# Kernel optimization log

Hardware: AMD Instinct MI355X
Metric: run time of the kernel (lower is better)

## Reference

```python
import jax, jax.numpy as jnp
import numpy as np

N_NODES = 100000
N_EDGES = 1600000
FEATURE = 128
HIDDEN = 128
CLASSES = 64


def _sage_conv(x, src, dst, W_l, b_l, W_r, num_nodes):
    # mean aggregation of source-node features at destination nodes
    msgs = x[src]                                            # [E, F]
    agg = jax.ops.segment_sum(msgs, dst, num_segments=num_nodes)   # [N, F]
    cnt = jax.ops.segment_sum(jnp.ones((src.shape[0],), x.dtype), dst,
                              num_segments=num_nodes)        # [N]
    mean = agg / jnp.maximum(cnt, 1.0)[:, None]              # zero for isolated nodes
    return mean @ W_l.T + b_l + x @ W_r.T


def setup_inputs() -> dict:
    key = jax.random.key(0)
    ks = jax.random.split(key, 8)
    x = jax.random.normal(ks[0], (N_NODES, FEATURE), dtype=jnp.float32)
    edge_index = jax.random.randint(ks[1], (2, N_EDGES), 0, N_NODES, dtype=jnp.int64)
    s1 = 1.0 / np.sqrt(FEATURE)
    s2 = 1.0 / np.sqrt(HIDDEN)
    W1l = jax.random.uniform(ks[2], (HIDDEN, FEATURE), jnp.float32, -s1, s1)
    b1l = jnp.zeros((HIDDEN,), jnp.float32)
    W1r = jax.random.uniform(ks[3], (HIDDEN, FEATURE), jnp.float32, -s1, s1)
    W2l = jax.random.uniform(ks[4], (CLASSES, HIDDEN), jnp.float32, -s2, s2)
    b2l = jnp.zeros((CLASSES,), jnp.float32)
    W2r = jax.random.uniform(ks[5], (CLASSES, HIDDEN), jnp.float32, -s2, s2)
    return {"x": x, "edge_index": edge_index,
            "W1l": W1l, "b1l": b1l, "W1r": W1r,
            "W2l": W2l, "b2l": b2l, "W2r": W2r}


def reference(x, edge_index, W1l, b1l, W1r, W2l, b2l, W2r):
    src, dst = edge_index[0], edge_index[1]
    h = _sage_conv(x, src, dst, W1l, b1l, W1r, N_NODES)
    h = jax.nn.relu(h)
    # F.dropout(training=False) is identity in eval mode
    out = _sage_conv(h, src, dst, W2l, b2l, W2r, N_NODES)
    return jax.nn.log_softmax(out, axis=1)
```

## Files before the change

### kernel.cpp

```cpp
#include <hip/hip_runtime.h>

#define NF 128
#define NC 64
#define NBA 640
#define NBKT 196

typedef short short8 __attribute__((ext_vector_type(8)));
typedef unsigned short ushort;
typedef float f32x4 __attribute__((ext_vector_type(4)));
typedef float f32x2 __attribute__((ext_vector_type(2)));
typedef unsigned int uint;
typedef unsigned char uchar;

__device__ __forceinline__ ushort f2b(float x) {
  unsigned u = __builtin_bit_cast(unsigned, x);
  u += 0x7fffu + ((u >> 16) & 1u);
  return (ushort)(u >> 16);
}

__global__ void prep_kernel(const float* __restrict__ x, ushort* __restrict__ xb,
                            uchar* __restrict__ x8, int n4, int nb_cast,
                            const float* __restrict__ W1l, const float* __restrict__ W1r,
                            ushort* __restrict__ Wp1,
                            const float* __restrict__ W2l, const float* __restrict__ W2r,
                            ushort* __restrict__ Wp2l, ushort* __restrict__ Wp2r) {
  int b = blockIdx.x;
  if (b < nb_cast) {
    int i = b * 256 + threadIdx.x;
    if (i >= n4) return;
    float4 v = ((const float4*)x)[i];
    ushort4 o;
    o.x = f2b(v.x); o.y = f2b(v.y); o.z = f2b(v.z); o.w = f2b(v.w);
    ((ushort4*)xb)[i] = o;
    int u = __builtin_amdgcn_cvt_pk_fp8_f32(v.x, v.y, 0, false);
    u = __builtin_amdgcn_cvt_pk_fp8_f32(v.z, v.w, u, true);
    ((uint*)x8)[i] = (uint)u;
  } else if (b < nb_cast + 128) {
    int tid = (b - nb_cast) * 256 + threadIdx.x;
    int j = tid & 7;
    int lane = (tid >> 3) & 63;
    int tile = tid >> 9;
    int nt = tile & 7, kt = tile >> 3;
    int k = kt * 32 + ((lane >> 4) << 3) + j;
    int n = nt * 16 + (lane & 15);
    float v = (k < 128) ? W1l[n * 128 + k] : W1r[n * 128 + (k - 128)];
    Wp1[tid] = f2b(v);
  } else {
    int tid0 = (b - nb_cast - 128) * 256 + threadIdx.x;
    int which = tid0 >> 13;
    int tid = tid0 & 8191;
    int j = tid & 7;
    int lane = (tid >> 3) & 63;
    int tile = tid >> 9;
    int nt = tile & 3, kt = tile >> 2;
    int k = kt * 32 + ((lane >> 4) << 3) + j;
    int n = nt * 16 + (lane & 15);
    const float* W = which ? W2r : W2l;
    ushort* Wp = which ? Wp2r : Wp2l;
    Wp[tid] = f2b(W[n * 128 + k]);
  }
}

__global__ __launch_bounds__(256) void bhistA_kernel(const int* __restrict__ dst,
                                                     int* __restrict__ cntA,
                                                     int nE, int epb) {
  __shared__ int lh[NBKT];
  const int t = threadIdx.x;
  for (int i = t; i < NBKT; i += 256) lh[i] = 0;
  __syncthreads();
  int s0 = blockIdx.x * epb, s1 = min(nE, s0 + epb);
  for (int e = s0 + t; e < s1; e += 256) atomicAdd(&lh[dst[e] >> 9], 1);
  __syncthreads();
  for (int i = t; i < NBKT; i += 256)
    cntA[(size_t)i * NBA + blockIdx.x] = lh[i];
}

__global__ __launch_bounds__(256) void scanL1_kernel(const int* __restrict__ in,
                                                     int* __restrict__ out,
                                                     int* __restrict__ bsum, int L) {
  const int t = threadIdx.x;
  const int base = blockIdx.x * 1024 + t * 4;
  int v[4];
  int tsum = 0;
#pragma unroll
  for (int k = 0; k < 4; ++k) {
    v[k] = (base + k < L) ? in[base + k] : 0;
    tsum += v[k];
  }
  int lane = t & 63, wid = t >> 6;
  int x = tsum;
#pragma unroll
  for (int d = 1; d < 64; d <<= 1) {
    int y = __shfl_up(x, d);
    if (lane >= d) x += y;
  }
  __shared__ int wsum[4];
  if (lane == 63) wsum[wid] = x;
  __syncthreads();
  int wbase = 0;
  for (int w = 0; w < wid; ++w) wbase += wsum[w];
  int run = wbase + x - tsum;
#pragma unroll
  for (int k = 0; k < 4; ++k) {
    if (base + k < L) out[base + k] = run;
    run += v[k];
  }
  if (t == 0) bsum[blockIdx.x] = wsum[0] + wsum[1] + wsum[2] + wsum[3];
}

__global__ void scanL2_kernel(int* __restrict__ bsum, int nb) {
  int lane = threadIdx.x;
  int i0 = 2 * lane, i1 = 2 * lane + 1;
  int v0 = (i0 < nb) ? bsum[i0] : 0;
  int v1 = (i1 < nb) ? bsum[i1] : 0;
  int s = v0 + v1;
  int x = s;
#pragma unroll
  for (int d = 1; d < 64; d <<= 1) {
    int y = __shfl_up(x, d);
    if (lane >= d) x += y;
  }
  int ex = x - s;
  if (i0 < nb) bsum[i0] = ex;
  if (i1 < nb) bsum[i1] = ex + v0;
}

__global__ void scanL3_kernel(int* __restrict__ out, const int* __restrict__ bsum, int L) {
  int i = blockIdx.x * blockDim.x + threadIdx.x;
  if (i < L) out[i] += bsum[i >> 10];
}

__global__ __launch_bounds__(256) void bscatA_kernel(const int* __restrict__ src,
                                                     const int* __restrict__ dst,
                                                     const int* __restrict__ cntS,
                                                     uint* __restrict__ tmp,
                                                     int nE, int epb) {
  __shared__ int base[NBKT];
  __shared__ int cur[NBKT];
  const int t = threadIdx.x;
  for (int i = t; i < NBKT; i += 256) {
    base[i] = cntS[(size_t)i * NBA + blockIdx.x];
    cur[i] = 0;
  }
  __syncthreads();
  int s0 = blockIdx.x * epb, s1 = min(nE, s0 + epb);
  for (int e = s0 + t; e < s1; e += 256) {
    int d = dst[e];
    int s = src[e];
    int b = d >> 9;
    int r = atomicAdd(&cur[b], 1);
    tmp[base[b] + r] = ((uint)(d & 511) << 17) | (uint)s;
  }
}

__global__ __launch_bounds__(256) void bsortB_kernel(const uint* __restrict__ tmp,
                                                     const int* __restrict__ cntS,
                                                     int* __restrict__ esrc,
                                                     int* __restrict__ deg,
                                                     int* __restrict__ off,
                                                     int nN, int nE) {
  const int bkt = blockIdx.x;
  const int t = threadIdx.x;
  __shared__ int lh[512];
  __shared__ int cur[512];
  __shared__ int wsum[4];
  const int start = cntS[(size_t)bkt * NBA];
  const int end = (bkt + 1 < NBKT) ? cntS[(size_t)(bkt + 1) * NBA] : nE;
  lh[t] = 0;
  lh[t + 256] = 0;
  __syncthreads();
  for (int i = start + t; i < end; i += 256) {
    uint e = tmp[i];
    atomicAdd(&lh[e >> 17], 1);
  }
  __syncthreads();
  int v0 = lh[2 * t], v1 = lh[2 * t + 1];
  int ts = v0 + v1;
  int lane = t & 63, wid = t >> 6;
  int x = ts;
#pragma unroll
  for (int d = 1; d < 64; d <<= 1) {
    int y = __shfl_up(x, d);
    if (lane >= d) x += y;
  }
  if (lane == 63) wsum[wid] = x;
  __syncthreads();
  int wb = 0;
  for (int w = 0; w < wid; ++w) wb += wsum[w];
  int ex = wb + x - ts;
  cur[2 * t] = ex;
  cur[2 * t + 1] = ex + v0;
  int n0 = (bkt << 9) + 2 * t, n1 = n0 + 1;
  if (n0 < nN) { off[n0] = start + ex;      deg[n0] = v0; }
  if (n1 < nN) { off[n1] = start + ex + v0; deg[n1] = v1; }
  __syncthreads();
  for (int i = start + t; i < end; i += 256) {
    uint e = tmp[i];
    int r = atomicAdd(&cur[e >> 17], 1);
    esrc[start + r] = (int)(e & 0x1FFFFu);
  }
}

__global__ __launch_bounds__(256) void gather1_kernel(
    const uchar* __restrict__ x8, const int* __restrict__ esrc,
    const int* __restrict__ off, const int* __restrict__ deg,
    ushort* __restrict__ aggm, int nN) {
  const int w = (blockIdx.x * blockDim.x + threadIdx.x) >> 6;
  const int lane = threadIdx.x & 63;
  if (w >= nN) return;
  const int o = off[w];
  const int d = deg[w];
  const int g = lane >> 4;
  const int l = lane & 15;
  f32x2 acc[4] = {};
  int i = 0;
  for (; i + 8 <= d; i += 8) {
    int sA = esrc[o + i + g];
    int sB = esrc[o + i + 4 + g];
    uint2 vA = ((const uint2*)(x8 + (size_t)sA * NF))[l];
    uint2 vB = ((const uint2*)(x8 + (size_t)sB * NF))[l];
    acc[0] += __builtin_amdgcn_cvt_pk_f32_fp8(vA.x, false) +
              __builtin_amdgcn_cvt_pk_f32_fp8(vB.x, false);
    acc[1] += __builtin_amdgcn_cvt_pk_f32_fp8(vA.x, true) +
              __builtin_amdgcn_cvt_pk_f32_fp8(vB.x, true);
    acc[2] += __builtin_amdgcn_cvt_pk_f32_fp8(vA.y, false) +
              __builtin_amdgcn_cvt_pk_f32_fp8(vB.y, false);
    acc[3] += __builtin_amdgcn_cvt_pk_f32_fp8(vA.y, true) +
              __builtin_amdgcn_cvt_pk_f32_fp8(vB.y, true);
  }
  for (; i + 4 <= d; i += 4) {
    int s = esrc[o + i + g];
    uint2 v = ((const uint2*)(x8 + (size_t)s * NF))[l];
    acc[0] += __builtin_amdgcn_cvt_pk_f32_fp8(v.x, false);
    acc[1] += __builtin_amdgcn_cvt_pk_f32_fp8(v.x, true);
    acc[2] += __builtin_amdgcn_cvt_pk_f32_fp8(v.y, false);
    acc[3] += __builtin_amdgcn_cvt_pk_f32_fp8(v.y, true);
  }
  if (i + g < d) {
    int s = esrc[o + i + g];
    uint2 v = ((const uint2*)(x8 + (size_t)s * NF))[l];
    acc[0] += __builtin_amdgcn_cvt_pk_f32_fp8(v.x, false);
    acc[1] += __builtin_amdgcn_cvt_pk_f32_fp8(v.x, true);
    acc[2] += __builtin_amdgcn_cvt_pk_f32_fp8(v.y, false);
    acc[3] += __builtin_amdgcn_cvt_pk_f32_fp8(v.y, true);
  }
  float r[8];
#pragma unroll
  for (int k = 0; k < 4; ++k) { r[2 * k] = acc[k].x; r[2 * k + 1] = acc[k].y; }
#pragma unroll
  for (int k = 0; k < 8; ++k) {
    r[k] += __shfl_xor(r[k], 16);
    r[k] += __shfl_xor(r[k], 32);
  }
  if (g == 0) {
    float inv = 1.0f / fmaxf((float)d, 1.0f);
    uint4 ov;
    ov.x = (uint)f2b(r[0] * inv) | ((uint)f2b(r[1] * inv) << 16);
    ov.y = (uint)f2b(r[2] * inv) | ((uint)f2b(r[3] * inv) << 16);
    ov.z = (uint)f2b(r[4] * inv) | ((uint)f2b(r[5] * inv) << 16);
    ov.w = (uint)f2b(r[6] * inv) | ((uint)f2b(r[7] * inv) << 16);
    ((uint4*)(aggm + (size_t)w * NF))[l] = ov;
  }
}

__global__ __launch_bounds__(256) void gather2_kernel(
    const uchar* __restrict__ z8, const int* __restrict__ esrc,
    const int* __restrict__ off, const int* __restrict__ deg,
    float* __restrict__ aggz, int nN) {
  const int w = (blockIdx.x * blockDim.x + threadIdx.x) >> 6;
  const int lane = threadIdx.x & 63;
  if (w >= nN) return;
  const int o = off[w];
  const int d = deg[w];
  const int g = lane >> 4;
  const int l = lane & 15;
  f32x2 acc[2] = {};
  int i = 0;
  for (; i + 8 <= d; i += 8) {
    int sA = esrc[o + i + g];
    int sB = esrc[o + i + 4 + g];
    uint vA = ((const uint*)(z8 + (size_t)sA * NC))[l];
    uint vB = ((const uint*)(z8 + (size_t)sB * NC))[l];
    acc[0] += __builtin_amdgcn_cvt_pk_f32_fp8(vA, false) +
              __builtin_amdgcn_cvt_pk_f32_fp8(vB, false);
    acc[1] += __builtin_amdgcn_cvt_pk_f32_fp8(vA, true) +
              __builtin_amdgcn_cvt_pk_f32_fp8(vB, true);
  }
  for (; i + 4 <= d; i += 4) {
    int s = esrc[o + i + g];
    uint v = ((const uint*)(z8 + (size_t)s * NC))[l];
    acc[0] += __builtin_amdgcn_cvt_pk_f32_fp8(v, false);
    acc[1] += __builtin_amdgcn_cvt_pk_f32_fp8(v, true);
  }
  if (i + g < d) {
    int s = esrc[o + i + g];
    uint v = ((const uint*)(z8 + (size_t)s * NC))[l];
    acc[0] += __builtin_amdgcn_cvt_pk_f32_fp8(v, false);
    acc[1] += __builtin_amdgcn_cvt_pk_f32_fp8(v, true);
  }
  float r[4] = {acc[0].x, acc[0].y, acc[1].x, acc[1].y};
#pragma unroll
  for (int k = 0; k < 4; ++k) {
    r[k] += __shfl_xor(r[k], 16);
    r[k] += __shfl_xor(r[k], 32);
  }
  if (g == 0) {
    float inv = 1.0f / fmaxf((float)d, 1.0f);
    ((float4*)(aggz + (size_t)w * NC))[l] =
        make_float4(r[0] * inv, r[1] * inv, r[2] * inv, r[3] * inv);
  }
}

__global__ __launch_bounds__(256) void layer1_mfma(
    const ushort* __restrict__ xb, const ushort* __restrict__ aggb,
    const ushort* __restrict__ Wp, const float* __restrict__ b1,
    ushort* __restrict__ hb, int nN) {
  const int t = threadIdx.x;
  const int wv = t >> 6;
  const int lane = t & 63;
  const int base = blockIdx.x * 64;
  __shared__ ushort As[64][264];
  for (int i = t; i < 64 * 32; i += 256) {
    int r = i >> 5, cq = i & 31;
    int node = base + r;
    short8 v = {};
    if (node < nN) {
      const ushort* sp = (cq < 16) ? (aggb + (size_t)node * NF + cq * 8)
                                   : (xb + (size_t)node * NF + (cq - 16) * 8);
      v = *(const short8*)sp;
    }
    *(short8*)&As[r][cq * 8] = v;
  }
  __syncthreads();

  f32x4 acc[8] = {};
  const int arow = wv * 16 + (lane & 15);
  const int kq = (lane >> 4) * 8;
#pragma unroll
  for (int kt = 0; kt < 8; ++kt) {
    short8 af = *(const short8*)&As[arow][kt * 32 + kq];
#pragma unroll
    for (int nt = 0; nt < 8; ++nt) {
      short8 bf = *(const short8*)(Wp + ((size_t)(kt * 8 + nt) * 64 + lane) * 8);
      acc[nt] = __builtin_amdgcn_mfma_f32_16x16x32_bf16(af, bf, acc[nt], 0, 0, 0);
    }
  }
  const int quad = lane >> 4;
  const int cl = lane & 15;
#pragma unroll
  for (int nt = 0; nt < 8; ++nt) {
    float bj = b1[nt * 16 + cl];
#pragma unroll
    for (int r = 0; r < 4; ++r) {
      int node = base + wv * 16 + quad * 4 + r;
      if (node < nN) {
        float vv = fmaxf(acc[nt][r] + bj, 0.0f);
        hb[(size_t)node * NF + nt * 16 + cl] = f2b(vv);
      }
    }
  }
}

__global__ __launch_bounds__(256) void layer2a_mfma(
    const ushort* __restrict__ hb, const ushort* __restrict__ Wp,
    uchar* __restrict__ z8, int nN) {
  const int t = threadIdx.x;
  const int wv = t >> 6;
  const int lane = t & 63;
  const int base = blockIdx.x * 64;
  __shared__ ushort As[64][136];
  for (int i = t; i < 64 * 16; i += 256) {
    int r = i >> 4, cq = i & 15;
    int node = base + r;
    short8 v = {};
    if (node < nN) v = *(const short8*)(hb + (size_t)node * NF + cq * 8);
    *(short8*)&As[r][cq * 8] = v;
  }
  __syncthreads();

  f32x4 acc[4] = {};
  const int arow = wv * 16 + (lane & 15);
  const int kq = (lane >> 4) * 8;
#pragma unroll
  for (int kt = 0; kt < 4; ++kt) {
    short8 af = *(const short8*)&As[arow][kt * 32 + kq];
#pragma unroll
    for (int nt = 0; nt < 4; ++nt) {
      short8 bf = *(const short8*)(Wp + ((size_t)(kt * 4 + nt) * 64 + lane) * 8);
      acc[nt] = __builtin_amdgcn_mfma_f32_16x16x32_bf16(af, bf, acc[nt], 0, 0, 0);
    }
  }
  const int quad = lane >> 4;
  const int cl = lane & 15;
#pragma unroll
  for (int r = 0; r < 4; ++r) {
    int node = base + wv * 16 + quad * 4 + r;
    if (node < nN) {
      int u = __builtin_amdgcn_cvt_pk_fp8_f32(acc[0][r], acc[1][r], 0, false);
      u = __builtin_amdgcn_cvt_pk_fp8_f32(acc[2][r], acc[3][r], u, true);
      ((uint*)(z8 + (size_t)node * NC))[cl] = (uint)u;
    }
  }
}

__global__ __launch_bounds__(256) void layer2b_mfma(
    const ushort* __restrict__ hb, const float* __restrict__ aggz,
    const ushort* __restrict__ Wp, const float* __restrict__ b2,
    float* __restrict__ out, int nN) {
  const int t = threadIdx.x;
  const int wv = t >> 6;
  const int lane = t & 63;
  const int base = blockIdx.x * 64;
  __shared__ ushort As[64][136];
  for (int i = t; i < 64 * 16; i += 256) {
    int r = i >> 4, cq = i & 15;
    int node = base + r;
    short8 v = {};
    if (node < nN) v = *(const short8*)(hb + (size_t)node * NF + cq * 8);
    *(short8*)&As[r][cq * 8] = v;
  }
  __syncthreads();

  f32x4 acc[4] = {};
  const int arow = wv * 16 + (lane & 15);
  const int kq = (lane >> 4) * 8;
#pragma unroll
  for (int kt = 0; kt < 4; ++kt) {
    short8 af = *(const short8*)&As[arow][kt * 32 + kq];
#pragma unroll
    for (int nt = 0; nt < 4; ++nt) {
      short8 bf = *(const short8*)(Wp + ((size_t)(kt * 4 + nt) * 64 + lane) * 8);
      acc[nt] = __builtin_amdgcn_mfma_f32_16x16x32_bf16(af, bf, acc[nt], 0, 0, 0);
    }
  }
  const int quad = lane >> 4;
  const int cl = lane & 15;
  float bj[4];
#pragma unroll
  for (int nt = 0; nt < 4; ++nt) bj[nt] = b2[nt * 16 + cl];

#pragma unroll
  for (int r = 0; r < 4; ++r) {
    int node = base + wv * 16 + quad * 4 + r;
    int nvalid = (node < nN);
    float a0 = 0.f, a1 = 0.f, a2 = 0.f, a3 = 0.f;
    if (nvalid) {
      float4 av = ((const float4*)(aggz + (size_t)node * NC))[cl];
      a0 = av.x; a1 = av.y; a2 = av.z; a3 = av.w;
    }
    float v0 = acc[0][r] + bj[0] + a0;
    float v1 = acc[1][r] + bj[1] + a1;
    float v2 = acc[2][r] + bj[2] + a2;
    float v3 = acc[3][r] + bj[3] + a3;
    float mx = fmaxf(fmaxf(v0, v1), fmaxf(v2, v3));
#pragma unroll
    for (int s = 1; s < 16; s <<= 1) mx = fmaxf(mx, __shfl_xor(mx, s));
    float sm = expf(v0 - mx) + expf(v1 - mx) + expf(v2 - mx) + expf(v3 - mx);
#pragma unroll
    for (int s = 1; s < 16; s <<= 1) sm += __shfl_xor(sm, s);
    float ls = mx + logf(sm);
    if (nvalid) {
      float* op = out + (size_t)node * NC;
      op[0 * 16 + cl] = v0 - ls;
      op[1 * 16 + cl] = v1 - ls;
      op[2 * 16 + cl] = v2 - ls;
      op[3 * 16 + cl] = v3 - ls;
    }
  }
}

extern "C" void kernel_launch(void* const* d_in, const int* in_sizes, int n_in,
                              void* d_out, int out_size, void* d_ws, size_t ws_size,
                              hipStream_t stream) {
  const float* x   = (const float*)d_in[0];
  const int*   ei  = (const int*)d_in[1];
  const float* W1l = (const float*)d_in[2];
  const float* b1l = (const float*)d_in[3];
  const float* W1r = (const float*)d_in[4];
  const float* W2l = (const float*)d_in[5];
  const float* b2l = (const float*)d_in[6];
  const float* W2r = (const float*)d_in[7];
  float* out = (float*)d_out;

  const int nN = in_sizes[0] / NF;
  const int nE = in_sizes[1] / 2;
  const int* src = ei;
  const int* dst = ei + nE;

  char* p = (char*)d_ws;
  ushort* xb   = (ushort*)p; p += (size_t)nN * NF * 2;
  ushort* hb   = (ushort*)p; p += (size_t)nN * NF * 2;
  ushort* aggb = (ushort*)p; p += (size_t)nN * NF * 2;
  ushort* Wp1  = (ushort*)p; p += 256 * 128 * 2;
  ushort* Wp2l = (ushort*)p; p += 128 * 64 * 2;
  ushort* Wp2r = (ushort*)p; p += 128 * 64 * 2;
  int* cntA = (int*)p; p += (size_t)NBKT * NBA * 4;
  int* cntS = (int*)p; p += (size_t)NBKT * NBA * 4;
  int* bsum = (int*)p; p += 512;
  int* deg  = (int*)p; p += (size_t)nN * 4;
  int* off  = (int*)p; p += (size_t)nN * 4;
  int* esrc = (int*)p; p += (size_t)nE * 4;
  uint* tmp = (uint*)p; p += (size_t)nE * 4;

  uchar* x8   = (uchar*)hb;
  uchar* z8   = (uchar*)tmp;
  float* aggz = (float*)aggb;

  const int n4 = nN * NF / 4;
  const int nb_cast = (n4 + 255) / 256;
  const int epb = (nE + NBA - 1) / NBA;
  const int L = NBKT * NBA;
  const int nbL = (L + 1023) / 1024;

  prep_kernel<<<nb_cast + 128 + 64, 256, 0, stream>>>(x, xb, x8, n4, nb_cast,
                                                      W1l, W1r, Wp1,
                                                      W2l, W2r, Wp2l, Wp2r);

  bhistA_kernel<<<NBA, 256, 0, stream>>>(dst, cntA, nE, epb);
  scanL1_kernel<<<nbL, 256, 0, stream>>>(cntA, cntS, bsum, L);
  scanL2_kernel<<<1, 64, 0, stream>>>(bsum, nbL);
  scanL3_kernel<<<(L + 255) / 256, 256, 0, stream>>>(cntS, bsum, L);
  bscatA_kernel<<<NBA, 256, 0, stream>>>(src, dst, cntS, tmp, nE, epb);
  bsortB_kernel<<<NBKT, 256, 0, stream>>>(tmp, cntS, esrc, deg, off, nN, nE);

  gather1_kernel<<<(nN + 3) / 4, 256, 0, stream>>>(x8, esrc, off, deg, aggb, nN);
  layer1_mfma<<<(nN + 63) / 64, 256, 0, stream>>>(xb, aggb, Wp1, b1l, hb, nN);

  layer2a_mfma<<<(nN + 63) / 64, 256, 0, stream>>>(hb, Wp2l, z8, nN);
  gather2_kernel<<<(nN + 3) / 4, 256, 0, stream>>>(z8, esrc, off, deg, aggz, nN);
  layer2b_mfma<<<(nN + 63) / 64, 256, 0, stream>>>(hb, aggz, Wp2r, b2l, out, nN);
}
```

Baseline: 316.7 us.

## Fuse histogram into prep, fold scan fixup, widen gathers, fuse layer1 with layer2a

The bucket histogram now runs as extra blocks of the prep kernel. The final scan-add kernel is removed and its block offsets are added where bscatA and bsortB read them. Layer 1 and the layer-2 left projection are fused: the ReLU output is written into LDS and reused for the second MFMA, so hb is not re-read from global memory. Both gather kernels now use 8 lanes per row with wider loads and 16 edges per iteration. Together these cut launch count and global traffic, at the cost of more registers, one extra shuffle stage per reduction, and more shared state in the prep kernel.

```diff
diff --git a/kernel.cpp b/kernel.cpp
--- a/kernel.cpp
+++ b/kernel.cpp
@@ -18,12 +18,15 @@
   return (ushort)(u >> 16);
 }
 
-__global__ void prep_kernel(const float* __restrict__ x, ushort* __restrict__ xb,
-                            uchar* __restrict__ x8, int n4, int nb_cast,
-                            const float* __restrict__ W1l, const float* __restrict__ W1r,
-                            ushort* __restrict__ Wp1,
-                            const float* __restrict__ W2l, const float* __restrict__ W2r,
-                            ushort* __restrict__ Wp2l, ushort* __restrict__ Wp2r) {
+__global__ __launch_bounds__(256) void prep_kernel(
+    const float* __restrict__ x, ushort* __restrict__ xb,
+    uchar* __restrict__ x8, int n4, int nb_cast,
+    const float* __restrict__ W1l, const float* __restrict__ W1r,
+    ushort* __restrict__ Wp1,
+    const float* __restrict__ W2l, const float* __restrict__ W2r,
+    ushort* __restrict__ Wp2l, ushort* __restrict__ Wp2r,
+    const int* __restrict__ dst, int* __restrict__ cntA, int nE, int epb) {
+  __shared__ int lh[NBKT];
   int b = blockIdx.x;
   if (b < nb_cast) {
     int i = b * 256 + threadIdx.x;
@@ -45,7 +48,7 @@
     int n = nt * 16 + (lane & 15);
     float v = (k < 128) ? W1l[n * 128 + k] : W1r[n * 128 + (k - 128)];
     Wp1[tid] = f2b(v);
-  } else {
+  } else if (b < nb_cast + 192) {
     int tid0 = (b - nb_cast - 128) * 256 + threadIdx.x;
     int which = tid0 >> 13;
     int tid = tid0 & 8191;
@@ -58,21 +61,17 @@
     const float* W = which ? W2r : W2l;
     ushort* Wp = which ? Wp2r : Wp2l;
     Wp[tid] = f2b(W[n * 128 + k]);
-  }
-}
-
-__global__ __launch_bounds__(256) void bhistA_kernel(const int* __restrict__ dst,
-                                                     int* __restrict__ cntA,
-                                                     int nE, int epb) {
-  __shared__ int lh[NBKT];
-  const int t = threadIdx.x;
-  for (int i = t; i < NBKT; i += 256) lh[i] = 0;
-  __syncthreads();
-  int s0 = blockIdx.x * epb, s1 = min(nE, s0 + epb);
-  for (int e = s0 + t; e < s1; e += 256) atomicAdd(&lh[dst[e] >> 9], 1);
-  __syncthreads();
-  for (int i = t; i < NBKT; i += 256)
-    cntA[(size_t)i * NBA + blockIdx.x] = lh[i];
+  } else {
+    int blk = b - nb_cast - 192;
+    const int t = threadIdx.x;
+    for (int i = t; i < NBKT; i += 256) lh[i] = 0;
+    __syncthreads();
+    int s0 = blk * epb, s1 = min(nE, s0 + epb);
+    for (int e = s0 + t; e < s1; e += 256) atomicAdd(&lh[dst[e] >> 9], 1);
+    __syncthreads();
+    for (int i = t; i < NBKT; i += 256)
+      cntA[(size_t)i * NBA + blk] = lh[i];
+  }
 }
 
 __global__ __launch_bounds__(256) void scanL1_kernel(const int* __restrict__ in,
@@ -125,21 +124,18 @@
   if (i1 < nb) bsum[i1] = ex + v0;
 }
 
-__global__ void scanL3_kernel(int* __restrict__ out, const int* __restrict__ bsum, int L) {
-  int i = blockIdx.x * blockDim.x + threadIdx.x;
-  if (i < L) out[i] += bsum[i >> 10];
-}
-
 __global__ __launch_bounds__(256) void bscatA_kernel(const int* __restrict__ src,
                                                      const int* __restrict__ dst,
                                                      const int* __restrict__ cntS,
+                                                     const int* __restrict__ bsum,
                                                      uint* __restrict__ tmp,
                                                      int nE, int epb) {
   __shared__ int base[NBKT];
   __shared__ int cur[NBKT];
   const int t = threadIdx.x;
   for (int i = t; i < NBKT; i += 256) {
-    base[i] = cntS[(size_t)i * NBA + blockIdx.x];
+    size_t idx = (size_t)i * NBA + blockIdx.x;
+    base[i] = cntS[idx] + bsum[idx >> 10];
     cur[i] = 0;
   }
   __syncthreads();
@@ -155,6 +151,7 @@
 
 __global__ __launch_bounds__(256) void bsortB_kernel(const uint* __restrict__ tmp,
                                                      const int* __restrict__ cntS,
+                                                     const int* __restrict__ bsum,
                                                      int* __restrict__ esrc,
                                                      int* __restrict__ deg,
                                                      int* __restrict__ off,
@@ -164,8 +161,15 @@
   __shared__ int lh[512];
   __shared__ int cur[512];
   __shared__ int wsum[4];
-  const int start = cntS[(size_t)bkt * NBA];
-  const int end = (bkt + 1 < NBKT) ? cntS[(size_t)(bkt + 1) * NBA] : nE;
+  const size_t ia = (size_t)bkt * NBA;
+  const int start = cntS[ia] + bsum[ia >> 10];
+  int end;
+  if (bkt + 1 < NBKT) {
+    const size_t ib = (size_t)(bkt + 1) * NBA;
+    end = cntS[ib] + bsum[ib >> 10];
+  } else {
+    end = nE;
+  }
   lh[t] = 0;
   lh[t + 256] = 0;
   __syncthreads();
@@ -210,15 +214,15 @@
   if (w >= nN) return;
   const int o = off[w];
   const int d = deg[w];
-  const int g = lane >> 4;
-  const int l = lane & 15;
-  f32x2 acc[4] = {};
+  const int g = lane >> 3;
+  const int l = lane & 7;
+  f32x2 acc[8] = {};
   int i = 0;
-  for (; i + 8 <= d; i += 8) {
+  for (; i + 16 <= d; i += 16) {
     int sA = esrc[o + i + g];
-    int sB = esrc[o + i + 4 + g];
-    uint2 vA = ((const uint2*)(x8 + (size_t)sA * NF))[l];
-    uint2 vB = ((const uint2*)(x8 + (size_t)sB * NF))[l];
+    int sB = esrc[o + i + 8 + g];
+    uint4 vA = ((const uint4*)(x8 + (size_t)sA * NF))[l];
+    uint4 vB = ((const uint4*)(x8 + (size_t)sB * NF))[l];
     acc[0] += __builtin_amdgcn_cvt_pk_f32_fp8(vA.x, false) +
               __builtin_amdgcn_cvt_pk_f32_fp8(vB.x, false);
     acc[1] += __builtin_amdgcn_cvt_pk_f32_fp8(vA.x, true) +
@@ -227,39 +231,61 @@
               __builtin_amdgcn_cvt_pk_f32_fp8(vB.y, false);
     acc[3] += __builtin_amdgcn_cvt_pk_f32_fp8(vA.y, true) +
               __builtin_amdgcn_cvt_pk_f32_fp8(vB.y, true);
-  }
-  for (; i + 4 <= d; i += 4) {
+    acc[4] += __builtin_amdgcn_cvt_pk_f32_fp8(vA.z, false) +
+              __builtin_amdgcn_cvt_pk_f32_fp8(vB.z, false);
+    acc[5] += __builtin_amdgcn_cvt_pk_f32_fp8(vA.z, true) +
+              __builtin_amdgcn_cvt_pk_f32_fp8(vB.z, true);
+    acc[6] += __builtin_amdgcn_cvt_pk_f32_fp8(vA.w, false) +
+              __builtin_amdgcn_cvt_pk_f32_fp8(vB.w, false);
+    acc[7] += __builtin_amdgcn_cvt_pk_f32_fp8(vA.w, true) +
+              __builtin_amdgcn_cvt_pk_f32_fp8(vB.w, true);
+  }
+  for (; i + 8 <= d; i += 8) {
     int s = esrc[o + i + g];
-    uint2 v = ((const uint2*)(x8 + (size_t)s * NF))[l];
+    uint4 v = ((const uint4*)(x8 + (size_t)s * NF))[l];
     acc[0] += __builtin_amdgcn_cvt_pk_f32_fp8(v.x, false);
     acc[1] += __builtin_amdgcn_cvt_pk_f32_fp8(v.x, true);
     acc[2] += __builtin_amdgcn_cvt_pk_f32_fp8(v.y, false);
     acc[3] += __builtin_amdgcn_cvt_pk_f32_fp8(v.y, true);
+    acc[4] += __builtin_amdgcn_cvt_pk_f32_fp8(v.z, false);
+    acc[5] += __builtin_amdgcn_cvt_pk_f32_fp8(v.z, true);
+    acc[6] += __builtin_amdgcn_cvt_pk_f32_fp8(v.w, false);
+    acc[7] += __builtin_amdgcn_cvt_pk_f32_fp8(v.w, true);
   }
   if (i + g < d) {
     int s = esrc[o + i + g];
-    uint2 v = ((const uint2*)(x8 + (size_t)s * NF))[l];
+    uint4 v = ((const uint4*)(x8 + (size_t)s * NF))[l];
     acc[0] += __builtin_amdgcn_cvt_pk_f32_fp8(v.x, false);
     acc[1] += __builtin_amdgcn_cvt_pk_f32_fp8(v.x, true);
     acc[2] += __builtin_amdgcn_cvt_pk_f32_fp8(v.y, false);
     acc[3] += __builtin_amdgcn_cvt_pk_f32_fp8(v.y, true);
-  }
-  float r[8];
-#pragma unroll
-  for (int k = 0; k < 4; ++k) { r[2 * k] = acc[k].x; r[2 * k + 1] = acc[k].y; }
-#pragma unroll
-  for (int k = 0; k < 8; ++k) {
+    acc[4] += __builtin_amdgcn_cvt_pk_f32_fp8(v.z, false);
+    acc[5] += __builtin_amdgcn_cvt_pk_f32_fp8(v.z, true);
+    acc[6] += __builtin_amdgcn_cvt_pk_f32_fp8(v.w, false);
+    acc[7] += __builtin_amdgcn_cvt_pk_f32_fp8(v.w, true);
+  }
+  float r[16];
+#pragma unroll
+  for (int k = 0; k < 8; ++k) { r[2 * k] = acc[k].x; r[2 * k + 1] = acc[k].y; }
+#pragma unroll
+  for (int k = 0; k < 16; ++k) {
+    r[k] += __shfl_xor(r[k], 8);
     r[k] += __shfl_xor(r[k], 16);
     r[k] += __shfl_xor(r[k], 32);
   }
   if (g == 0) {
     float inv = 1.0f / fmaxf((float)d, 1.0f);
-    uint4 ov;
-    ov.x = (uint)f2b(r[0] * inv) | ((uint)f2b(r[1] * inv) << 16);
-    ov.y = (uint)f2b(r[2] * inv) | ((uint)f2b(r[3] * inv) << 16);
-    ov.z = (uint)f2b(r[4] * inv) | ((uint)f2b(r[5] * inv) << 16);
-    ov.w = (uint)f2b(r[6] * inv) | ((uint)f2b(r[7] * inv) << 16);
-    ((uint4*)(aggm + (size_t)w * NF))[l] = ov;
+    uint4 o0, o1;
+    o0.x = (uint)f2b(r[0] * inv)  | ((uint)f2b(r[1] * inv) << 16);
+    o0.y = (uint)f2b(r[2] * inv)  | ((uint)f2b(r[3] * inv) << 16);
+    o0.z = (uint)f2b(r[4] * inv)  | ((uint)f2b(r[5] * inv) << 16);
+    o0.w = (uint)f2b(r[6] * inv)  | ((uint)f2b(r[7] * inv) << 16);
+    o1.x = (uint)f2b(r[8] * inv)  | ((uint)f2b(r[9] * inv) << 16);
+    o1.y = (uint)f2b(r[10] * inv) | ((uint)f2b(r[11] * inv) << 16);
+    o1.z = (uint)f2b(r[12] * inv) | ((uint)f2b(r[13] * inv) << 16);
+    o1.w = (uint)f2b(r[14] * inv) | ((uint)f2b(r[15] * inv) << 16);
+    ((uint4*)(aggm + (size_t)w * NF))[2 * l] = o0;
+    ((uint4*)(aggm + (size_t)w * NF))[2 * l + 1] = o1;
   }
 }
 
@@ -272,49 +298,62 @@
   if (w >= nN) return;
   const int o = off[w];
   const int d = deg[w];
-  const int g = lane >> 4;
-  const int l = lane & 15;
-  f32x2 acc[2] = {};
+  const int g = lane >> 3;
+  const int l = lane & 7;
+  f32x2 acc[4] = {};
   int i = 0;
+  for (; i + 16 <= d; i += 16) {
+    int sA = esrc[o + i + g];
+    int sB = esrc[o + i + 8 + g];
+    uint2 vA = ((const uint2*)(z8 + (size_t)sA * NC))[l];
+    uint2 vB = ((const uint2*)(z8 + (size_t)sB * NC))[l];
+    acc[0] += __builtin_amdgcn_cvt_pk_f32_fp8(vA.x, false) +
+              __builtin_amdgcn_cvt_pk_f32_fp8(vB.x, false);
+    acc[1] += __builtin_amdgcn_cvt_pk_f32_fp8(vA.x, true) +
+              __builtin_amdgcn_cvt_pk_f32_fp8(vB.x, true);
+    acc[2] += __builtin_amdgcn_cvt_pk_f32_fp8(vA.y, false) +
+              __builtin_amdgcn_cvt_pk_f32_fp8(vB.y, false);
+    acc[3] += __builtin_amdgcn_cvt_pk_f32_fp8(vA.y, true) +
+              __builtin_amdgcn_cvt_pk_f32_fp8(vB.y, true);
+  }
   for (; i + 8 <= d; i += 8) {
-    int sA = esrc[o + i + g];
-    int sB = esrc[o + i + 4 + g];
-    uint vA = ((const uint*)(z8 + (size_t)sA * NC))[l];
-    uint vB = ((const uint*)(z8 + (size_t)sB * NC))[l];
-    acc[0] += __builtin_amdgcn_cvt_pk_f32_fp8(vA, false) +
-              __builtin_amdgcn_cvt_pk_f32_fp8(vB, false);
-    acc[1] += __builtin_amdgcn_cvt_pk_f32_fp8(vA, true) +
-              __builtin_amdgcn_cvt_pk_f32_fp8(vB, true);
-  }
-  for (; i + 4 <= d; i += 4) {
     int s = esrc[o + i + g];
-    uint v = ((const uint*)(z8 + (size_t)s * NC))[l];
-    acc[0] += __builtin_amdgcn_cvt_pk_f32_fp8(v, false);
-    acc[1] += __builtin_amdgcn_cvt_pk_f32_fp8(v, true);
+    uint2 v = ((const uint2*)(z8 + (size_t)s * NC))[l];
+    acc[0] += __builtin_amdgcn_cvt_pk_f32_fp8(v.x, false);
+    acc[1] += __builtin_amdgcn_cvt_pk_f32_fp8(v.x, true);
+    acc[2] += __builtin_amdgcn_cvt_pk_f32_fp8(v.y, false);
+    acc[3] += __builtin_amdgcn_cvt_pk_f32_fp8(v.y, true);
   }
   if (i + g < d) {
     int s = esrc[o + i + g];
-    uint v = ((const uint*)(z8 + (size_t)s * NC))[l];
-    acc[0] += __builtin_amdgcn_cvt_pk_f32_fp8(v, false);
-    acc[1] += __builtin_amdgcn_cvt_pk_f32_fp8(v, true);
-  }
-  float r[4] = {acc[0].x, acc[0].y, acc[1].x, acc[1].y};
-#pragma unroll
-  for (int k = 0; k < 4; ++k) {
+    uint2 v = ((const uint2*)(z8 + (size_t)s * NC))[l];
+    acc[0] += __builtin_amdgcn_cvt_pk_f32_fp8(v.x, false);
+    acc[1] += __builtin_amdgcn_cvt_pk_f32_fp8(v.x, true);
+    acc[2] += __builtin_amdgcn_cvt_pk_f32_fp8(v.y, false);
+    acc[3] += __builtin_amdgcn_cvt_pk_f32_fp8(v.y, true);
+  }
+  float r[8] = {acc[0].x, acc[0].y, acc[1].x, acc[1].y,
+                acc[2].x, acc[2].y, acc[3].x, acc[3].y};
+#pragma unroll
+  for (int k = 0; k < 8; ++k) {
+    r[k] += __shfl_xor(r[k], 8);
     r[k] += __shfl_xor(r[k], 16);
     r[k] += __shfl_xor(r[k], 32);
   }
   if (g == 0) {
     float inv = 1.0f / fmaxf((float)d, 1.0f);
-    ((float4*)(aggz + (size_t)w * NC))[l] =
+    ((float4*)(aggz + (size_t)w * NC))[2 * l] =
         make_float4(r[0] * inv, r[1] * inv, r[2] * inv, r[3] * inv);
-  }
-}
-
-__global__ __launch_bounds__(256) void layer1_mfma(
+    ((float4*)(aggz + (size_t)w * NC))[2 * l + 1] =
+        make_float4(r[4] * inv, r[5] * inv, r[6] * inv, r[7] * inv);
+  }
+}
+
+__global__ __launch_bounds__(256) void layer12_mfma(
     const ushort* __restrict__ xb, const ushort* __restrict__ aggb,
-    const ushort* __restrict__ Wp, const float* __restrict__ b1,
-    ushort* __restrict__ hb, int nN) {
+    const ushort* __restrict__ Wp1, const float* __restrict__ b1,
+    const ushort* __restrict__ Wp2l,
+    ushort* __restrict__ hb, uchar* __restrict__ z8, int nN) {
   const int t = threadIdx.x;
   const int wv = t >> 6;
   const int lane = t & 63;
@@ -341,7 +380,7 @@
     short8 af = *(const short8*)&As[arow][kt * 32 + kq];
 #pragma unroll
     for (int nt = 0; nt < 8; ++nt) {
-      short8 bf = *(const short8*)(Wp + ((size_t)(kt * 8 + nt) * 64 + lane) * 8);
+      short8 bf = *(const short8*)(Wp1 + ((size_t)(kt * 8 + nt) * 64 + lane) * 8);
       acc[nt] = __builtin_amdgcn_mfma_f32_16x16x32_bf16(af, bf, acc[nt], 0, 0, 0);
     }
   }
@@ -353,51 +392,28 @@
 #pragma unroll
     for (int r = 0; r < 4; ++r) {
       int node = base + wv * 16 + quad * 4 + r;
-      if (node < nN) {
-        float vv = fmaxf(acc[nt][r] + bj, 0.0f);
-        hb[(size_t)node * NF + nt * 16 + cl] = f2b(vv);
-      }
-    }
-  }
-}
-
-__global__ __launch_bounds__(256) void layer2a_mfma(
-    const ushort* __restrict__ hb, const ushort* __restrict__ Wp,
-    uchar* __restrict__ z8, int nN) {
-  const int t = threadIdx.x;
-  const int wv = t >> 6;
-  const int lane = t & 63;
-  const int base = blockIdx.x * 64;
-  __shared__ ushort As[64][136];
-  for (int i = t; i < 64 * 16; i += 256) {
-    int r = i >> 4, cq = i & 15;
-    int node = base + r;
-    short8 v = {};
-    if (node < nN) v = *(const short8*)(hb + (size_t)node * NF + cq * 8);
-    *(short8*)&As[r][cq * 8] = v;
-  }
-  __syncthreads();
-
-  f32x4 acc[4] = {};
-  const int arow = wv * 16 + (lane & 15);
-  const int kq = (lane >> 4) * 8;
+      ushort hv = f2b(fmaxf(acc[nt][r] + bj, 0.0f));
+      As[wv * 16 + quad * 4 + r][nt * 16 + cl] = hv;
+      if (node < nN) hb[(size_t)node * NF + nt * 16 + cl] = hv;
+    }
+  }
+
+  f32x4 acc2[4] = {};
 #pragma unroll
   for (int kt = 0; kt < 4; ++kt) {
     short8 af = *(const short8*)&As[arow][kt * 32 + kq];
 #pragma unroll
     for (int nt = 0; nt < 4; ++nt) {
-      short8 bf = *(const short8*)(Wp + ((size_t)(kt * 4 + nt) * 64 + lane) * 8);
-      acc[nt] = __builtin_amdgcn_mfma_f32_16x16x32_bf16(af, bf, acc[nt], 0, 0, 0);
-    }
-  }
-  const int quad = lane >> 4;
-  const int cl = lane & 15;
+      short8 bf = *(const short8*)(Wp2l + ((size_t)(kt * 4 + nt) * 64 + lane) * 8);
+      acc2[nt] = __builtin_amdgcn_mfma_f32_16x16x32_bf16(af, bf, acc2[nt], 0, 0, 0);
+    }
+  }
 #pragma unroll
   for (int r = 0; r < 4; ++r) {
     int node = base + wv * 16 + quad * 4 + r;
     if (node < nN) {
-      int u = __builtin_amdgcn_cvt_pk_fp8_f32(acc[0][r], acc[1][r], 0, false);
-      u = __builtin_amdgcn_cvt_pk_fp8_f32(acc[2][r], acc[3][r], u, true);
+      int u = __builtin_amdgcn_cvt_pk_fp8_f32(acc2[0][r], acc2[1][r], 0, false);
+      u = __builtin_amdgcn_cvt_pk_fp8_f32(acc2[2][r], acc2[3][r], u, true);
       ((uint*)(z8 + (size_t)node * NC))[cl] = (uint)u;
     }
   }
@@ -512,21 +528,18 @@
   const int L = NBKT * NBA;
   const int nbL = (L + 1023) / 1024;
 
-  prep_kernel<<<nb_cast + 128 + 64, 256, 0, stream>>>(x, xb, x8, n4, nb_cast,
-                                                      W1l, W1r, Wp1,
-                                                      W2l, W2r, Wp2l, Wp2r);
-
-  bhistA_kernel<<<NBA, 256, 0, stream>>>(dst, cntA, nE, epb);
+  prep_kernel<<<nb_cast + 192 + NBA, 256, 0, stream>>>(
+      x, xb, x8, n4, nb_cast, W1l, W1r, Wp1, W2l, W2r, Wp2l, Wp2r,
+      dst, cntA, nE, epb);
+
   scanL1_kernel<<<nbL, 256, 0, stream>>>(cntA, cntS, bsum, L);
   scanL2_kernel<<<1, 64, 0, stream>>>(bsum, nbL);
-  scanL3_kernel<<<(L + 255) / 256, 256, 0, stream>>>(cntS, bsum, L);
-  bscatA_kernel<<<NBA, 256, 0, stream>>>(src, dst, cntS, tmp, nE, epb);
-  bsortB_kernel<<<NBKT, 256, 0, stream>>>(tmp, cntS, esrc, deg, off, nN, nE);
+  bscatA_kernel<<<NBA, 256, 0, stream>>>(src, dst, cntS, bsum, tmp, nE, epb);
+  bsortB_kernel<<<NBKT, 256, 0, stream>>>(tmp, cntS, bsum, esrc, deg, off, nN, nE);
 
   gather1_kernel<<<(nN + 3) / 4, 256, 0, stream>>>(x8, esrc, off, deg, aggb, nN);
-  layer1_mfma<<<(nN + 63) / 64, 256, 0, stream>>>(xb, aggb, Wp1, b1l, hb, nN);
-
-  layer2a_mfma<<<(nN + 63) / 64, 256, 0, stream>>>(hb, Wp2l, z8, nN);
+  layer12_mfma<<<(nN + 63) / 64, 256, 0, stream>>>(xb, aggb, Wp1, b1l, Wp2l, hb, z8, nN);
+
   gather2_kernel<<<(nN + 3) / 4, 256, 0, stream>>>(z8, esrc, off, deg, aggz, nN);
   layer2b_mfma<<<(nN + 63) / 64, 256, 0, stream>>>(hb, aggz, Wp2r, b2l, out, nN);
 }
```

Measured after the change: 298.4 us. -5.8%, faster.
